# Kernel tuning notes

Measured on AMD Instinct MI355X. Metric: run time of the kernel, lower is better.

The kernel has to match this reference:

```python
import jax, jax.numpy as jnp
import numpy as np

B, R = 4096, 2048

def setup_inputs() -> dict:
    key = jax.random.key(0)
    twist_batch = jax.random.normal(key, (B, R, 3), dtype=jnp.float32)
    return {"twist_batch": twist_batch}

def _rodrigues(twist_batch):
    # twist_batch: [B, R, 3]
    # rot_angle: clamp(||w||, 1e-5)
    rot_angle = jnp.maximum(jnp.linalg.norm(twist_batch, axis=2, keepdims=True), 1e-5)  # [B,R,1]
    axis = twist_batch / rot_angle  # [B,R,3]
    a0, a1, a2 = axis[..., 0], axis[..., 1], axis[..., 2]
    o = jnp.zeros_like(a0)
    # skew-symmetric cross-product matrix A: [B,R,3,3]
    A = jnp.stack([o, -a2, a1,
                   a2, o, -a0,
                   -a1, a0, o], axis=-1).reshape(*a0.shape, 3, 3)
    s = jnp.sin(rot_angle)[..., None]          # [B,R,1,1]
    c1 = (1.0 - jnp.cos(rot_angle))[..., None]  # [B,R,1,1]
    AA = jnp.matmul(A, A)                       # batched 3x3 mm
    I = jnp.eye(3, dtype=twist_batch.dtype)
    return I + A * s + AA * c1  # [B,R,3,3]

def reference(twist_batch):
    return _rodrigues(twist_batch)
```

## Files before the change

kernel.cpp:

```cpp
#include <hip/hip_runtime.h>
#include <math.h>


typedef float v4f __attribute__((ext_vector_type(4)));

#define TPB 256
#define RPT 4
#define RPB (TPB * RPT)
#define IN_F4 (RPB * 3 / 4)
#define OUT_F4 (RPB * 9 / 4)

__global__ __launch_bounds__(TPB) void twist2mat_kernel(
    const v4f* __restrict__ in4, v4f* __restrict__ out4) {
    const int tid = threadIdx.x;
    const int bin  = blockIdx.x * IN_F4;
    const int bout = blockIdx.x * OUT_F4;

    __shared__ v4f buf[OUT_F4];

#pragma unroll
    for (int k = 0; k < 3; ++k)
        buf[tid + TPB * k] = __builtin_nontemporal_load(&in4[bin + tid + TPB * k]);
    __syncthreads();

    const v4f x0 = buf[3 * tid + 0];
    const v4f x1 = buf[3 * tid + 1];
    const v4f x2 = buf[3 * tid + 2];
    __syncthreads();

    const float w[12] = {x0.x, x0.y, x0.z, x0.w,
                         x1.x, x1.y, x1.z, x1.w,
                         x2.x, x2.y, x2.z, x2.w};
    float o[36];
#pragma unroll
    for (int j = 0; j < 4; ++j) {
        const float w0 = w[3 * j], w1 = w[3 * j + 1], w2 = w[3 * j + 2];
        const float n2  = fmaf(w0, w0, fmaf(w1, w1, w2 * w2));
        const float t   = fmaxf(sqrtf(n2), 1e-5f);
        const float inv = 1.0f / t;
        const float a0 = w0 * inv, a1 = w1 * inv, a2 = w2 * inv;
        float s, c;
        __sincosf(t, &s, &c);
        const float c1 = 1.0f - c;
        const float aa = fmaf(a0, a0, fmaf(a1, a1, a2 * a2));
        float* r = &o[9 * j];
        r[0] = fmaf(c1, fmaf(a0, a0, -aa), 1.0f);
        r[1] = fmaf(c1, a0 * a1, -s * a2);
        r[2] = fmaf(c1, a0 * a2,  s * a1);
        r[3] = fmaf(c1, a0 * a1,  s * a2);
        r[4] = fmaf(c1, fmaf(a1, a1, -aa), 1.0f);
        r[5] = fmaf(c1, a1 * a2, -s * a0);
        r[6] = fmaf(c1, a0 * a2, -s * a1);
        r[7] = fmaf(c1, a1 * a2,  s * a0);
        r[8] = fmaf(c1, fmaf(a2, a2, -aa), 1.0f);
    }

#pragma unroll
    for (int k = 0; k < 9; ++k) {
        v4f v = {o[4 * k + 0], o[4 * k + 1], o[4 * k + 2], o[4 * k + 3]};
        buf[9 * tid + k] = v;
    }
    __syncthreads();

#pragma unroll
    for (int k = 0; k < 9; ++k)
        __builtin_nontemporal_store(buf[tid + TPB * k],
                                    &out4[bout + tid + TPB * k]);
}

extern "C" void kernel_launch(void* const* d_in, const int* in_sizes, int n_in,
                              void* d_out, int out_size, void* d_ws, size_t ws_size,
                              hipStream_t stream) {
    (void)n_in; (void)out_size; (void)d_ws; (void)ws_size;
    const v4f* in4 = (const v4f*)d_in[0];
    v4f* out4 = (v4f*)d_out;
    const int nrot = in_sizes[0] / 3;
    const int grid = nrot / RPB;
    twist2mat_kernel<<<grid, TPB, 0, stream>>>(in4, out4);
}
```

Before: 354.9 us.

## Process one rotation per thread with smaller blocks and higher occupancy

Each thread now handles one rotation instead of four, so a 256-thread block covers 256 rotations and the grid is four times larger. The launch bounds request 8 blocks per CU, and shared memory per block shrinks. This aims to raise occupancy and memory-level parallelism for a bandwidth-bound kernel. In exchange, each thread does fewer bytes of work, the LDS traffic is now scalar floats, which may cause bank conflicts, and some global loads and stores are predicated.

```diff
diff --git a/kernel.cpp b/kernel.cpp
--- a/kernel.cpp
+++ b/kernel.cpp
@@ -5,67 +5,57 @@
 typedef float v4f __attribute__((ext_vector_type(4)));
 
 #define TPB 256
-#define RPT 4
-#define RPB (TPB * RPT)
+#define RPB TPB
 #define IN_F4 (RPB * 3 / 4)
 #define OUT_F4 (RPB * 9 / 4)
 
-__global__ __launch_bounds__(TPB) void twist2mat_kernel(
+__global__ __launch_bounds__(TPB, 8) void twist2mat_kernel(
     const v4f* __restrict__ in4, v4f* __restrict__ out4) {
     const int tid = threadIdx.x;
     const int bin  = blockIdx.x * IN_F4;
     const int bout = blockIdx.x * OUT_F4;
 
     __shared__ v4f buf[OUT_F4];
+    float* fbuf = (float*)buf;
 
-#pragma unroll
-    for (int k = 0; k < 3; ++k)
-        buf[tid + TPB * k] = __builtin_nontemporal_load(&in4[bin + tid + TPB * k]);
+    if (tid < IN_F4)
+        buf[tid] = __builtin_nontemporal_load(&in4[bin + tid]);
     __syncthreads();
 
-    const v4f x0 = buf[3 * tid + 0];
-    const v4f x1 = buf[3 * tid + 1];
-    const v4f x2 = buf[3 * tid + 2];
+    const float w0 = fbuf[3 * tid + 0];
+    const float w1 = fbuf[3 * tid + 1];
+    const float w2 = fbuf[3 * tid + 2];
     __syncthreads();
 
-    const float w[12] = {x0.x, x0.y, x0.z, x0.w,
-                         x1.x, x1.y, x1.z, x1.w,
-                         x2.x, x2.y, x2.z, x2.w};
-    float o[36];
-#pragma unroll
-    for (int j = 0; j < 4; ++j) {
-        const float w0 = w[3 * j], w1 = w[3 * j + 1], w2 = w[3 * j + 2];
-        const float n2  = fmaf(w0, w0, fmaf(w1, w1, w2 * w2));
-        const float t   = fmaxf(sqrtf(n2), 1e-5f);
-        const float inv = 1.0f / t;
-        const float a0 = w0 * inv, a1 = w1 * inv, a2 = w2 * inv;
-        float s, c;
-        __sincosf(t, &s, &c);
-        const float c1 = 1.0f - c;
-        const float aa = fmaf(a0, a0, fmaf(a1, a1, a2 * a2));
-        float* r = &o[9 * j];
-        r[0] = fmaf(c1, fmaf(a0, a0, -aa), 1.0f);
-        r[1] = fmaf(c1, a0 * a1, -s * a2);
-        r[2] = fmaf(c1, a0 * a2,  s * a1);
-        r[3] = fmaf(c1, a0 * a1,  s * a2);
-        r[4] = fmaf(c1, fmaf(a1, a1, -aa), 1.0f);
-        r[5] = fmaf(c1, a1 * a2, -s * a0);
-        r[6] = fmaf(c1, a0 * a2, -s * a1);
-        r[7] = fmaf(c1, a1 * a2,  s * a0);
-        r[8] = fmaf(c1, fmaf(a2, a2, -aa), 1.0f);
-    }
-
-#pragma unroll
-    for (int k = 0; k < 9; ++k) {
-        v4f v = {o[4 * k + 0], o[4 * k + 1], o[4 * k + 2], o[4 * k + 3]};
-        buf[9 * tid + k] = v;
-    }
-    __syncthreads();
+    const float n2  = fmaf(w0, w0, fmaf(w1, w1, w2 * w2));
+    const float t   = fmaxf(sqrtf(n2), 1e-5f);
+    const float inv = 1.0f / t;
+    const float a0 = w0 * inv, a1 = w1 * inv, a2 = w2 * inv;
+    float s, c;
+    __sincosf(t, &s, &c);
+    const float c1 = 1.0f - c;
+    const float aa = fmaf(a0, a0, fmaf(a1, a1, a2 * a2));
+    float r[9];
+    r[0] = fmaf(c1, fmaf(a0, a0, -aa), 1.0f);
+    r[1] = fmaf(c1, a0 * a1, -s * a2);
+    r[2] = fmaf(c1, a0 * a2,  s * a1);
+    r[3] = fmaf(c1, a0 * a1,  s * a2);
+    r[4] = fmaf(c1, fmaf(a1, a1, -aa), 1.0f);
+    r[5] = fmaf(c1, a1 * a2, -s * a0);
+    r[6] = fmaf(c1, a0 * a2, -s * a1);
+    r[7] = fmaf(c1, a1 * a2,  s * a0);
+    r[8] = fmaf(c1, fmaf(a2, a2, -aa), 1.0f);
 
 #pragma unroll
     for (int k = 0; k < 9; ++k)
-        __builtin_nontemporal_store(buf[tid + TPB * k],
-                                    &out4[bout + tid + TPB * k]);
+        fbuf[9 * tid + k] = r[k];
+    __syncthreads();
+
+    __builtin_nontemporal_store(buf[tid          ], &out4[bout + tid          ]);
+    __builtin_nontemporal_store(buf[tid + TPB    ], &out4[bout + tid + TPB    ]);
+    if (tid < OUT_F4 - 2 * TPB)
+        __builtin_nontemporal_store(buf[tid + 2 * TPB],
+                                    &out4[bout + tid + 2 * TPB]);
 }
 
 extern "C" void kernel_launch(void* const* d_in, const int* in_sizes, int n_in,
```

Result: faster. 346.4 us (-2.4%).

## Use persistent per-wave tiles with register prefetch and wave-local LDS transpose

Applied to the files above, without the earlier changes.

Replaces the one-block-per-tile launch with a fixed grid of 1024 persistent blocks. Each wave owns its own tiles and loops over them, prefetching the next tile's input into registers while it computes the current one. Block-wide __syncthreads are replaced by wave-local LDS fences, and inputs are read directly with strided non-LDS loads. This is meant to hide load latency and cut barrier and launch overhead, at the cost of uncoalesced 3-float4 strided loads, non-nontemporal input reads, and possible tail imbalance.

```diff
diff --git a/kernel.cpp b/kernel.cpp
--- a/kernel.cpp
+++ b/kernel.cpp
@@ -5,67 +5,83 @@
 typedef float v4f __attribute__((ext_vector_type(4)));
 
 #define TPB 256
-#define RPT 4
-#define RPB (TPB * RPT)
-#define IN_F4 (RPB * 3 / 4)
-#define OUT_F4 (RPB * 9 / 4)
+#define NWAVE (TPB / 64)
+#define T_IN 192
+#define T_OUT 576
+#define GRID 1024
 
-__global__ __launch_bounds__(TPB) void twist2mat_kernel(
-    const v4f* __restrict__ in4, v4f* __restrict__ out4) {
-    const int tid = threadIdx.x;
-    const int bin  = blockIdx.x * IN_F4;
-    const int bout = blockIdx.x * OUT_F4;
+#define WAVE_LDS_FENCE()                                      \
+    do {                                                      \
+        asm volatile("s_waitcnt lgkmcnt(0)" ::: "memory");    \
+        __builtin_amdgcn_sched_barrier(0);                    \
+    } while (0)
 
-    __shared__ v4f buf[OUT_F4];
+__global__ __launch_bounds__(TPB, 4) void twist2mat_kernel(
+    const v4f* __restrict__ in4, v4f* __restrict__ out4, const int ntiles) {
+    __shared__ v4f buf[NWAVE][T_OUT];
+    const int wid  = threadIdx.x >> 6;
+    const int lane = threadIdx.x & 63;
+    v4f* wbuf = buf[wid];
+    const int nw = GRID * NWAVE;
+
+    int tile = blockIdx.x * NWAVE + wid;
+    if (tile >= ntiles) return;
+
+    v4f x0 = in4[tile * T_IN + 3 * lane + 0];
+    v4f x1 = in4[tile * T_IN + 3 * lane + 1];
+    v4f x2 = in4[tile * T_IN + 3 * lane + 2];
+
+    for (; tile < ntiles; tile += nw) {
+        const float w[12] = {x0.x, x0.y, x0.z, x0.w,
+                             x1.x, x1.y, x1.z, x1.w,
+                             x2.x, x2.y, x2.z, x2.w};
+
+        const int nt = tile + nw;
+        if (nt < ntiles) {
+            x0 = in4[nt * T_IN + 3 * lane + 0];
+            x1 = in4[nt * T_IN + 3 * lane + 1];
+            x2 = in4[nt * T_IN + 3 * lane + 2];
+        }
+
+        float o[36];
+#pragma unroll
+        for (int j = 0; j < 4; ++j) {
+            const float w0 = w[3 * j], w1 = w[3 * j + 1], w2 = w[3 * j + 2];
+            const float n2  = fmaf(w0, w0, fmaf(w1, w1, w2 * w2));
+            const float t   = fmaxf(sqrtf(n2), 1e-5f);
+            const float inv = 1.0f / t;
+            const float a0 = w0 * inv, a1 = w1 * inv, a2 = w2 * inv;
+            float s, c;
+            __sincosf(t, &s, &c);
+            const float c1 = 1.0f - c;
+            const float aa = fmaf(a0, a0, fmaf(a1, a1, a2 * a2));
+            float* r = &o[9 * j];
+            r[0] = fmaf(c1, fmaf(a0, a0, -aa), 1.0f);
+            r[1] = fmaf(c1, a0 * a1, -s * a2);
+            r[2] = fmaf(c1, a0 * a2,  s * a1);
+            r[3] = fmaf(c1, a0 * a1,  s * a2);
+            r[4] = fmaf(c1, fmaf(a1, a1, -aa), 1.0f);
+            r[5] = fmaf(c1, a1 * a2, -s * a0);
+            r[6] = fmaf(c1, a0 * a2, -s * a1);
+            r[7] = fmaf(c1, a1 * a2,  s * a0);
+            r[8] = fmaf(c1, fmaf(a2, a2, -aa), 1.0f);
+        }
+
+        WAVE_LDS_FENCE();
 
 #pragma unroll
-    for (int k = 0; k < 3; ++k)
-        buf[tid + TPB * k] = __builtin_nontemporal_load(&in4[bin + tid + TPB * k]);
-    __syncthreads();
+        for (int k = 0; k < 9; ++k) {
+            v4f v = {o[4 * k + 0], o[4 * k + 1], o[4 * k + 2], o[4 * k + 3]};
+            wbuf[9 * lane + k] = v;
+        }
 
-    const v4f x0 = buf[3 * tid + 0];
-    const v4f x1 = buf[3 * tid + 1];
-    const v4f x2 = buf[3 * tid + 2];
-    __syncthreads();
-
-    const float w[12] = {x0.x, x0.y, x0.z, x0.w,
-                         x1.x, x1.y, x1.z, x1.w,
-                         x2.x, x2.y, x2.z, x2.w};
-    float o[36];
-#pragma unroll
-    for (int j = 0; j < 4; ++j) {
-        const float w0 = w[3 * j], w1 = w[3 * j + 1], w2 = w[3 * j + 2];
-        const float n2  = fmaf(w0, w0, fmaf(w1, w1, w2 * w2));
-        const float t   = fmaxf(sqrtf(n2), 1e-5f);
-        const float inv = 1.0f / t;
-        const float a0 = w0 * inv, a1 = w1 * inv, a2 = w2 * inv;
-        float s, c;
-        __sincosf(t, &s, &c);
-        const float c1 = 1.0f - c;
-        const float aa = fmaf(a0, a0, fmaf(a1, a1, a2 * a2));
-        float* r = &o[9 * j];
-        r[0] = fmaf(c1, fmaf(a0, a0, -aa), 1.0f);
-        r[1] = fmaf(c1, a0 * a1, -s * a2);
-        r[2] = fmaf(c1, a0 * a2,  s * a1);
-        r[3] = fmaf(c1, a0 * a1,  s * a2);
-        r[4] = fmaf(c1, fmaf(a1, a1, -aa), 1.0f);
-        r[5] = fmaf(c1, a1 * a2, -s * a0);
-        r[6] = fmaf(c1, a0 * a2, -s * a1);
-        r[7] = fmaf(c1, a1 * a2,  s * a0);
-        r[8] = fmaf(c1, fmaf(a2, a2, -aa), 1.0f);
-    }
+        WAVE_LDS_FENCE();
 
 #pragma unroll
-    for (int k = 0; k < 9; ++k) {
-        v4f v = {o[4 * k + 0], o[4 * k + 1], o[4 * k + 2], o[4 * k + 3]};
-        buf[9 * tid + k] = v;
+        for (int k = 0; k < 9; ++k)
+            __builtin_nontemporal_store(wbuf[lane + 64 * k],
+                                        &out4[tile * T_OUT + lane + 64 * k]);
     }
-    __syncthreads();
-
-#pragma unroll
-    for (int k = 0; k < 9; ++k)
-        __builtin_nontemporal_store(buf[tid + TPB * k],
-                                    &out4[bout + tid + TPB * k]);
 }
 
 extern "C" void kernel_launch(void* const* d_in, const int* in_sizes, int n_in,
@@ -75,6 +91,6 @@
     const v4f* in4 = (const v4f*)d_in[0];
     v4f* out4 = (v4f*)d_out;
     const int nrot = in_sizes[0] / 3;
-    const int grid = nrot / RPB;
-    twist2mat_kernel<<<grid, TPB, 0, stream>>>(in4, out4);
+    const int ntiles = nrot / 256;
+    twist2mat_kernel<<<GRID, TPB, 0, stream>>>(in4, out4, ntiles);
 }
```

After: 367.6 us. 3.6% more time.
